# Optimization experiments

Measured on AMD Instinct MI355X. Metric: run time of the kernel, lower is better.

Reference implementation:

```python
import jax, jax.numpy as jnp
import numpy as np

T, B, N, E = 16384, 64, 1_000_000, 4096  # steps, per-step batch, train samples, eval dim


def setup_inputs() -> dict:
    key = jax.random.key(0)
    k1, k2, k3 = jax.random.split(key, 3)
    indices = jax.random.randint(k1, (T, B), 0, N, dtype=jnp.int64)
    M_prev = jax.random.normal(k2, (E,), dtype=jnp.float32)
    # torch module initializes params to zeros; use small random values so the
    # affine recurrence exercises nontrivial math without blowing up.
    params = jax.random.normal(k3, (N, 2), dtype=jnp.float32) * 0.01
    return {"indices": indices, "M_prev": M_prev, "params": params}


def reference(indices, M_prev, params):
    # Per-step gather + sum: alpha_t = sum(params[idx_t, 0]), beta_t = sum(params[idx_t, 1])
    coeffs = params[indices].sum(axis=1)          # [T, 2]
    alpha, beta = coeffs[:, 0], coeffs[:, 1]      # [T], [T]

    # Affine recurrence M_t = alpha_t * M_{t-1} + beta_t as a parallel scan:
    # compose (a1,b1) then (a2,b2) -> (a2*a1, a2*b1 + b2)
    def compose(c1, c2):
        a1, b1 = c1
        a2, b2 = c2
        return a2 * a1, a2 * b1 + b2

    A, Bc = jax.lax.associative_scan(compose, (alpha, beta))  # prefix affine maps
    # M_t = A_t * M_0 + B_t, broadcast over eval dim -> [T, E]
    return A[:, None] * M_prev[None, :] + Bc[:, None]
```

## Files before the change

kernel.cpp:

```cpp
#include <hip/hip_runtime.h>

#define T_DIM 16384
#define B_DIM 64
#define E_DIM 4096
#define NBLK  1024
#define CHUNK 16

typedef float f32x4 __attribute__((ext_vector_type(4)));

__global__ __launch_bounds__(256) void coeff_scan_kernel(
    const int*   __restrict__ indices,
    const float* __restrict__ params,
    float2*      __restrict__ lab,
    float2*      __restrict__ agg)
{
    __shared__ float sA[CHUNK], sB[CHUNK];
    const int tid   = threadIdx.x;
    const int lane  = tid & 63;
    const int wave  = tid >> 6;
    const int blk   = blockIdx.x;
    const int tbase = blk * CHUNK;
    const float2* __restrict__ P2 = (const float2*)params;

    const int j0 = wave * 4;
    int i0 = indices[((tbase + j0 + 0) << 6) + lane];
    int i1 = indices[((tbase + j0 + 1) << 6) + lane];
    int i2 = indices[((tbase + j0 + 2) << 6) + lane];
    int i3 = indices[((tbase + j0 + 3) << 6) + lane];
    float2 p0 = P2[i0], p1 = P2[i1], p2 = P2[i2], p3 = P2[i3];
    float a0 = p0.x, b0 = p0.y, a1 = p1.x, b1 = p1.y;
    float a2 = p2.x, b2 = p2.y, a3 = p3.x, b3 = p3.y;
    #pragma unroll
    for (int off = 32; off >= 1; off >>= 1) {
        a0 += __shfl_down(a0, off, 64);  b0 += __shfl_down(b0, off, 64);
        a1 += __shfl_down(a1, off, 64);  b1 += __shfl_down(b1, off, 64);
        a2 += __shfl_down(a2, off, 64);  b2 += __shfl_down(b2, off, 64);
        a3 += __shfl_down(a3, off, 64);  b3 += __shfl_down(b3, off, 64);
    }
    if (lane == 0) {
        sA[j0+0] = a0; sB[j0+0] = b0;
        sA[j0+1] = a1; sB[j0+1] = b1;
        sA[j0+2] = a2; sB[j0+2] = b2;
        sA[j0+3] = a3; sB[j0+3] = b3;
    }
    __syncthreads();

    if (tid == 0) {
        float a = 1.0f, b = 0.0f;
        #pragma unroll
        for (int j = 0; j < CHUNK; ++j) {
            float aj = sA[j], bj = sB[j];
            b = aj * b + bj;
            a = aj * a;
            sA[j] = a; sB[j] = b;
        }
        agg[blk] = make_float2(a, b);
    }
    __syncthreads();
    if (tid < CHUNK) lab[tbase + tid] = make_float2(sA[tid], sB[tid]);
}

__global__ __launch_bounds__(64) void scan_agg_kernel(
    const float2* __restrict__ agg,
    float2*       __restrict__ pref)
{
    const int lane = threadIdx.x;
    const int base = lane * 16;
    float ca[16], cb[16];
    float a = 1.0f, b = 0.0f;
    #pragma unroll
    for (int i = 0; i < 16; ++i) {
        float2 g = agg[base + i];
        b = g.x * b + g.y;
        a = g.x * a;
        ca[i] = a; cb[i] = b;
    }
    #pragma unroll
    for (int off = 1; off < 64; off <<= 1) {
        float pa = __shfl_up(a, off, 64);
        float pb = __shfl_up(b, off, 64);
        if (lane >= off) {
            float nb = a * pb + b;
            a = a * pa;
            b = nb;
        }
    }
    float ea = __shfl_up(a, 1, 64);
    float eb = __shfl_up(b, 1, 64);
    if (lane == 0) { ea = 1.0f; eb = 0.0f; }
    pref[base] = make_float2(ea, eb);
    #pragma unroll
    for (int i = 1; i < 16; ++i) {
        pref[base + i] = make_float2(ca[i-1] * ea, ca[i-1] * eb + cb[i-1]);
    }
}

__global__ __launch_bounds__(256) void out_kernel(
    const float2* __restrict__ lab,
    const float2* __restrict__ pref,
    const float*  __restrict__ M,
    float*        __restrict__ out)
{
    __shared__ float2 s[CHUNK];
    const int tid   = threadIdx.x;
    const int blk   = blockIdx.x;
    const int tbase = blk * CHUNK;
    if (tid < CHUNK) s[tid] = lab[tbase + tid];
    const float2 P = pref[blk];
    const f32x4* __restrict__ M4 = (const f32x4*)M;
    f32x4 m0 = M4[tid], m1 = M4[tid + 256], m2 = M4[tid + 512], m3 = M4[tid + 768];
    __syncthreads();
    #pragma unroll
    for (int j = 0; j < CHUNK; ++j) {
        const float la = s[j].x, lb = s[j].y;
        const float At = la * P.x;
        const float Bt = la * P.y + lb;
        f32x4* __restrict__ O4 = (f32x4*)(out + (size_t)(tbase + j) * E_DIM);
        f32x4 r;
        r = At * m0 + Bt;  __builtin_nontemporal_store(r, &O4[tid      ]);
        r = At * m1 + Bt;  __builtin_nontemporal_store(r, &O4[tid + 256]);
        r = At * m2 + Bt;  __builtin_nontemporal_store(r, &O4[tid + 512]);
        r = At * m3 + Bt;  __builtin_nontemporal_store(r, &O4[tid + 768]);
    }
}

extern "C" void kernel_launch(void* const* d_in, const int* in_sizes, int n_in,
                              void* d_out, int out_size, void* d_ws, size_t ws_size,
                              hipStream_t stream) {
    const int*   indices = (const int*)d_in[0];
    const float* M_prev  = (const float*)d_in[1];
    const float* params  = (const float*)d_in[2];
    float* out = (float*)d_out;

    float2* lab  = (float2*)d_ws;
    float2* agg  = lab + T_DIM;
    float2* pref = agg + NBLK;

    coeff_scan_kernel<<<NBLK, 256, 0, stream>>>(indices, params, lab, agg);
    scan_agg_kernel<<<1, 64, 0, stream>>>(agg, pref);
    out_kernel<<<NBLK, 256, 0, stream>>>(lab, pref, M_prev, out);
}
```

Baseline: 290.8 us.

## Fuse gather, scan and output into one kernel with decoupled lookback

Replaces the three-kernel pipeline with a single kernel. Each block publishes its chunk aggregate with a release flag, and wave 0 then scans all predecessor aggregates to get its prefix before writing its output rows. This removes two kernel launches and the workspace round trips for the local scan and prefix. The cost is a memset launch, per-block spin-waiting, and lookback work that grows linearly with the block index. It also relies on earlier blocks making forward progress while later ones wait.

```diff
diff --git a/kernel.cpp b/kernel.cpp
--- a/kernel.cpp
+++ b/kernel.cpp
@@ -8,40 +8,46 @@
 
 typedef float f32x4 __attribute__((ext_vector_type(4)));
 
-__global__ __launch_bounds__(256) void coeff_scan_kernel(
-    const int*   __restrict__ indices,
-    const float* __restrict__ params,
-    float2*      __restrict__ lab,
-    float2*      __restrict__ agg)
+__global__ __launch_bounds__(256) void fused_kernel(
+    const int*    __restrict__ indices,
+    const float*  __restrict__ params,
+    const float*  __restrict__ M,
+    float*        __restrict__ out,
+    float*        __restrict__ aggA,
+    float*        __restrict__ aggB,
+    unsigned int* __restrict__ flags)
 {
     __shared__ float sA[CHUNK], sB[CHUNK];
+    __shared__ float sP[2];
     const int tid   = threadIdx.x;
     const int lane  = tid & 63;
     const int wave  = tid >> 6;
     const int blk   = blockIdx.x;
     const int tbase = blk * CHUNK;
-    const float2* __restrict__ P2 = (const float2*)params;
 
-    const int j0 = wave * 4;
-    int i0 = indices[((tbase + j0 + 0) << 6) + lane];
-    int i1 = indices[((tbase + j0 + 1) << 6) + lane];
-    int i2 = indices[((tbase + j0 + 2) << 6) + lane];
-    int i3 = indices[((tbase + j0 + 3) << 6) + lane];
-    float2 p0 = P2[i0], p1 = P2[i1], p2 = P2[i2], p3 = P2[i3];
-    float a0 = p0.x, b0 = p0.y, a1 = p1.x, b1 = p1.y;
-    float a2 = p2.x, b2 = p2.y, a3 = p3.x, b3 = p3.y;
-    #pragma unroll
-    for (int off = 32; off >= 1; off >>= 1) {
-        a0 += __shfl_down(a0, off, 64);  b0 += __shfl_down(b0, off, 64);
-        a1 += __shfl_down(a1, off, 64);  b1 += __shfl_down(b1, off, 64);
-        a2 += __shfl_down(a2, off, 64);  b2 += __shfl_down(b2, off, 64);
-        a3 += __shfl_down(a3, off, 64);  b3 += __shfl_down(b3, off, 64);
-    }
-    if (lane == 0) {
-        sA[j0+0] = a0; sB[j0+0] = b0;
-        sA[j0+1] = a1; sB[j0+1] = b1;
-        sA[j0+2] = a2; sB[j0+2] = b2;
-        sA[j0+3] = a3; sB[j0+3] = b3;
+    {
+        const float2* __restrict__ P2 = (const float2*)params;
+        const int j0 = wave * 4;
+        int i0 = indices[((tbase + j0 + 0) << 6) + lane];
+        int i1 = indices[((tbase + j0 + 1) << 6) + lane];
+        int i2 = indices[((tbase + j0 + 2) << 6) + lane];
+        int i3 = indices[((tbase + j0 + 3) << 6) + lane];
+        float2 p0 = P2[i0], p1 = P2[i1], p2 = P2[i2], p3 = P2[i3];
+        float a0 = p0.x, b0 = p0.y, a1 = p1.x, b1 = p1.y;
+        float a2 = p2.x, b2 = p2.y, a3 = p3.x, b3 = p3.y;
+        #pragma unroll
+        for (int off = 32; off >= 1; off >>= 1) {
+            a0 += __shfl_down(a0, off, 64);  b0 += __shfl_down(b0, off, 64);
+            a1 += __shfl_down(a1, off, 64);  b1 += __shfl_down(b1, off, 64);
+            a2 += __shfl_down(a2, off, 64);  b2 += __shfl_down(b2, off, 64);
+            a3 += __shfl_down(a3, off, 64);  b3 += __shfl_down(b3, off, 64);
+        }
+        if (lane == 0) {
+            sA[j0+0] = a0; sB[j0+0] = b0;
+            sA[j0+1] = a1; sB[j0+1] = b1;
+            sA[j0+2] = a2; sB[j0+2] = b2;
+            sA[j0+3] = a3; sB[j0+3] = b3;
+        }
     }
     __syncthreads();
 
@@ -54,67 +60,58 @@
             a = aj * a;
             sA[j] = a; sB[j] = b;
         }
-        agg[blk] = make_float2(a, b);
+        __hip_atomic_store(&aggA[blk], a, __ATOMIC_RELAXED, __HIP_MEMORY_SCOPE_AGENT);
+        __hip_atomic_store(&aggB[blk], b, __ATOMIC_RELAXED, __HIP_MEMORY_SCOPE_AGENT);
+        __hip_atomic_store(&flags[blk], 1u, __ATOMIC_RELEASE, __HIP_MEMORY_SCOPE_AGENT);
+    }
+
+    const f32x4* __restrict__ M4 = (const f32x4*)M;
+    f32x4 m0 = M4[tid], m1 = M4[tid + 256], m2 = M4[tid + 512], m3 = M4[tid + 768];
+
+    if (wave == 0) {
+        float Pa = 1.0f, Pb = 0.0f;
+        const int npred   = blk;
+        const int nrounds = (npred + 63) >> 6;
+        for (int r = 0; r < nrounds; ++r) {
+            const int  idx = (r << 6) + lane;
+            const bool act = idx < npred;
+            const unsigned long long need = __ballot(act);
+            for (;;) {
+                unsigned int f = act
+                    ? __hip_atomic_load(&flags[idx], __ATOMIC_ACQUIRE, __HIP_MEMORY_SCOPE_AGENT)
+                    : 1u;
+                unsigned long long got = __ballot(f != 0u);
+                if ((got & need) == need) break;
+                __builtin_amdgcn_s_sleep(1);
+            }
+            float a = act ? __hip_atomic_load(&aggA[idx], __ATOMIC_RELAXED, __HIP_MEMORY_SCOPE_AGENT) : 1.0f;
+            float b = act ? __hip_atomic_load(&aggB[idx], __ATOMIC_RELAXED, __HIP_MEMORY_SCOPE_AGENT) : 0.0f;
+            #pragma unroll
+            for (int off = 1; off < 64; off <<= 1) {
+                float pa = __shfl_up(a, off, 64);
+                float pb = __shfl_up(b, off, 64);
+                if (lane >= off) {
+                    float nb = a * pb + b;
+                    a = a * pa;
+                    b = nb;
+                }
+            }
+            const float Sa = __shfl(a, 63, 64);
+            const float Sb = __shfl(b, 63, 64);
+            const float nPb = Sa * Pb + Sb;
+            Pa = Sa * Pa;
+            Pb = nPb;
+        }
+        if (lane == 0) { sP[0] = Pa; sP[1] = Pb; }
     }
     __syncthreads();
-    if (tid < CHUNK) lab[tbase + tid] = make_float2(sA[tid], sB[tid]);
-}
 
-__global__ __launch_bounds__(64) void scan_agg_kernel(
-    const float2* __restrict__ agg,
-    float2*       __restrict__ pref)
-{
-    const int lane = threadIdx.x;
-    const int base = lane * 16;
-    float ca[16], cb[16];
-    float a = 1.0f, b = 0.0f;
-    #pragma unroll
-    for (int i = 0; i < 16; ++i) {
-        float2 g = agg[base + i];
-        b = g.x * b + g.y;
-        a = g.x * a;
-        ca[i] = a; cb[i] = b;
-    }
-    #pragma unroll
-    for (int off = 1; off < 64; off <<= 1) {
-        float pa = __shfl_up(a, off, 64);
-        float pb = __shfl_up(b, off, 64);
-        if (lane >= off) {
-            float nb = a * pb + b;
-            a = a * pa;
-            b = nb;
-        }
-    }
-    float ea = __shfl_up(a, 1, 64);
-    float eb = __shfl_up(b, 1, 64);
-    if (lane == 0) { ea = 1.0f; eb = 0.0f; }
-    pref[base] = make_float2(ea, eb);
-    #pragma unroll
-    for (int i = 1; i < 16; ++i) {
-        pref[base + i] = make_float2(ca[i-1] * ea, ca[i-1] * eb + cb[i-1]);
-    }
-}
-
-__global__ __launch_bounds__(256) void out_kernel(
-    const float2* __restrict__ lab,
-    const float2* __restrict__ pref,
-    const float*  __restrict__ M,
-    float*        __restrict__ out)
-{
-    __shared__ float2 s[CHUNK];
-    const int tid   = threadIdx.x;
-    const int blk   = blockIdx.x;
-    const int tbase = blk * CHUNK;
-    if (tid < CHUNK) s[tid] = lab[tbase + tid];
-    const float2 P = pref[blk];
-    const f32x4* __restrict__ M4 = (const f32x4*)M;
-    f32x4 m0 = M4[tid], m1 = M4[tid + 256], m2 = M4[tid + 512], m3 = M4[tid + 768];
-    __syncthreads();
+    const float Pa = sP[0], Pb = sP[1];
     #pragma unroll
     for (int j = 0; j < CHUNK; ++j) {
-        const float la = s[j].x, lb = s[j].y;
-        const float At = la * P.x;
-        const float Bt = la * P.y + lb;
+        const float la = sA[j], lb = sB[j];
+        const float At = la * Pa;
+        const float Bt = la * Pb + lb;
         f32x4* __restrict__ O4 = (f32x4*)(out + (size_t)(tbase + j) * E_DIM);
         f32x4 r;
         r = At * m0 + Bt;  __builtin_nontemporal_store(r, &O4[tid      ]);
@@ -132,11 +129,12 @@
     const float* params  = (const float*)d_in[2];
     float* out = (float*)d_out;
 
-    float2* lab  = (float2*)d_ws;
-    float2* agg  = lab + T_DIM;
-    float2* pref = agg + NBLK;
+    float*        aggA  = (float*)d_ws;
+    float*        aggB  = aggA + NBLK;
+    unsigned int* flags = (unsigned int*)(aggB + NBLK);
 
-    coeff_scan_kernel<<<NBLK, 256, 0, stream>>>(indices, params, lab, agg);
-    scan_agg_kernel<<<1, 64, 0, stream>>>(agg, pref);
-    out_kernel<<<NBLK, 256, 0, stream>>>(lab, pref, M_prev, out);
+    hipMemsetAsync(flags, 0, NBLK * sizeof(unsigned int), stream);
+
+    fused_kernel<<<NBLK, 256, 0, stream>>>(indices, params, M_prev, out,
+                                           aggA, aggB, flags);
 }
```

Measured after the change: 353.0 us. +21.4%, slower.

## Fold block-aggregate scan into output kernel and vectorize index loads

Applied to the files above, without the earlier changes.

Removes the single-block scan_agg kernel. Each output block now recomputes its own exclusive prefix over the preceding block aggregates with a windowed wave scan, which saves one launch and its serial dependency. The coefficient kernel now loads indices as int4 per thread and reduces across 16 lanes instead of a full 64-lane shuffle reduction per row. The cost is redundant prefix work in later blocks, up to 16 windows of 64, which the first wave must finish before any stores begin.

```diff
diff --git a/kernel.cpp b/kernel.cpp
--- a/kernel.cpp
+++ b/kernel.cpp
@@ -16,105 +16,87 @@
 {
     __shared__ float sA[CHUNK], sB[CHUNK];
     const int tid   = threadIdx.x;
-    const int lane  = tid & 63;
-    const int wave  = tid >> 6;
     const int blk   = blockIdx.x;
     const int tbase = blk * CHUNK;
     const float2* __restrict__ P2 = (const float2*)params;
 
-    const int j0 = wave * 4;
-    int i0 = indices[((tbase + j0 + 0) << 6) + lane];
-    int i1 = indices[((tbase + j0 + 1) << 6) + lane];
-    int i2 = indices[((tbase + j0 + 2) << 6) + lane];
-    int i3 = indices[((tbase + j0 + 3) << 6) + lane];
-    float2 p0 = P2[i0], p1 = P2[i1], p2 = P2[i2], p3 = P2[i3];
-    float a0 = p0.x, b0 = p0.y, a1 = p1.x, b1 = p1.y;
-    float a2 = p2.x, b2 = p2.y, a3 = p3.x, b3 = p3.y;
+    const int4* __restrict__ I4 = (const int4*)(indices + tbase * B_DIM);
+    const int4 iv = I4[tid];
+    float2 g0 = P2[iv.x], g1 = P2[iv.y], g2 = P2[iv.z], g3 = P2[iv.w];
+    float a = (g0.x + g1.x) + (g2.x + g3.x);
+    float b = (g0.y + g1.y) + (g2.y + g3.y);
     #pragma unroll
-    for (int off = 32; off >= 1; off >>= 1) {
-        a0 += __shfl_down(a0, off, 64);  b0 += __shfl_down(b0, off, 64);
-        a1 += __shfl_down(a1, off, 64);  b1 += __shfl_down(b1, off, 64);
-        a2 += __shfl_down(a2, off, 64);  b2 += __shfl_down(b2, off, 64);
-        a3 += __shfl_down(a3, off, 64);  b3 += __shfl_down(b3, off, 64);
+    for (int off = 8; off >= 1; off >>= 1) {
+        a += __shfl_down(a, off, 64);
+        b += __shfl_down(b, off, 64);
     }
-    if (lane == 0) {
-        sA[j0+0] = a0; sB[j0+0] = b0;
-        sA[j0+1] = a1; sB[j0+1] = b1;
-        sA[j0+2] = a2; sB[j0+2] = b2;
-        sA[j0+3] = a3; sB[j0+3] = b3;
-    }
+    if ((tid & 15) == 0) { sA[tid >> 4] = a; sB[tid >> 4] = b; }
     __syncthreads();
 
     if (tid == 0) {
-        float a = 1.0f, b = 0.0f;
+        float A = 1.0f, B = 0.0f;
         #pragma unroll
         for (int j = 0; j < CHUNK; ++j) {
             float aj = sA[j], bj = sB[j];
-            b = aj * b + bj;
-            a = aj * a;
-            sA[j] = a; sB[j] = b;
+            B = aj * B + bj;
+            A = aj * A;
+            sA[j] = A; sB[j] = B;
         }
-        agg[blk] = make_float2(a, b);
+        agg[blk] = make_float2(A, B);
     }
     __syncthreads();
     if (tid < CHUNK) lab[tbase + tid] = make_float2(sA[tid], sB[tid]);
 }
 
-__global__ __launch_bounds__(64) void scan_agg_kernel(
-    const float2* __restrict__ agg,
-    float2*       __restrict__ pref)
-{
-    const int lane = threadIdx.x;
-    const int base = lane * 16;
-    float ca[16], cb[16];
-    float a = 1.0f, b = 0.0f;
-    #pragma unroll
-    for (int i = 0; i < 16; ++i) {
-        float2 g = agg[base + i];
-        b = g.x * b + g.y;
-        a = g.x * a;
-        ca[i] = a; cb[i] = b;
-    }
-    #pragma unroll
-    for (int off = 1; off < 64; off <<= 1) {
-        float pa = __shfl_up(a, off, 64);
-        float pb = __shfl_up(b, off, 64);
-        if (lane >= off) {
-            float nb = a * pb + b;
-            a = a * pa;
-            b = nb;
-        }
-    }
-    float ea = __shfl_up(a, 1, 64);
-    float eb = __shfl_up(b, 1, 64);
-    if (lane == 0) { ea = 1.0f; eb = 0.0f; }
-    pref[base] = make_float2(ea, eb);
-    #pragma unroll
-    for (int i = 1; i < 16; ++i) {
-        pref[base + i] = make_float2(ca[i-1] * ea, ca[i-1] * eb + cb[i-1]);
-    }
-}
-
 __global__ __launch_bounds__(256) void out_kernel(
     const float2* __restrict__ lab,
-    const float2* __restrict__ pref,
+    const float2* __restrict__ agg,
     const float*  __restrict__ M,
     float*        __restrict__ out)
 {
     __shared__ float2 s[CHUNK];
+    __shared__ float sP[2];
     const int tid   = threadIdx.x;
+    const int lane  = tid & 63;
     const int blk   = blockIdx.x;
     const int tbase = blk * CHUNK;
     if (tid < CHUNK) s[tid] = lab[tbase + tid];
-    const float2 P = pref[blk];
+
     const f32x4* __restrict__ M4 = (const f32x4*)M;
     f32x4 m0 = M4[tid], m1 = M4[tid + 256], m2 = M4[tid + 512], m3 = M4[tid + 768];
+
+    if (tid < 64) {
+        float Xa = 1.0f, Xb = 0.0f;
+        const int nwin = (blk + 63) >> 6;
+        for (int w = 0; w < nwin; ++w) {
+            const int idx = (w << 6) + lane;
+            float a = 1.0f, b = 0.0f;
+            if (idx < blk) { float2 g = agg[idx]; a = g.x; b = g.y; }
+            #pragma unroll
+            for (int off = 1; off < 64; off <<= 1) {
+                const float pa = __shfl_up(a, off, 64);
+                const float pb = __shfl_up(b, off, 64);
+                if (lane >= off) {
+                    const float nb = a * pb + b;
+                    a = a * pa;
+                    b = nb;
+                }
+            }
+            const float Sa = __shfl(a, 63, 64);
+            const float Sb = __shfl(b, 63, 64);
+            Xb = Sa * Xb + Sb;
+            Xa = Sa * Xa;
+        }
+        if (lane == 0) { sP[0] = Xa; sP[1] = Xb; }
+    }
     __syncthreads();
+
+    const float Pa = sP[0], Pb = sP[1];
     #pragma unroll
     for (int j = 0; j < CHUNK; ++j) {
         const float la = s[j].x, lb = s[j].y;
-        const float At = la * P.x;
-        const float Bt = la * P.y + lb;
+        const float At = la * Pa;
+        const float Bt = la * Pb + lb;
         f32x4* __restrict__ O4 = (f32x4*)(out + (size_t)(tbase + j) * E_DIM);
         f32x4 r;
         r = At * m0 + Bt;  __builtin_nontemporal_store(r, &O4[tid      ]);
@@ -132,11 +114,9 @@
     const float* params  = (const float*)d_in[2];
     float* out = (float*)d_out;
 
-    float2* lab  = (float2*)d_ws;
-    float2* agg  = lab + T_DIM;
-    float2* pref = agg + NBLK;
+    float2* lab = (float2*)d_ws;
+    float2* agg = lab + T_DIM;
 
     coeff_scan_kernel<<<NBLK, 256, 0, stream>>>(indices, params, lab, agg);
-    scan_agg_kernel<<<1, 64, 0, stream>>>(agg, pref);
-    out_kernel<<<NBLK, 256, 0, stream>>>(lab, pref, M_prev, out);
+    out_kernel<<<NBLK, 256, 0, stream>>>(lab, agg, M_prev, out);
 }
```

Result: no change. 289.5 us (-0.4%).
